# Optimization experiments

Hardware: AMD Instinct MI355X
Metric: run time of the kernel (lower is better)

Reference implementation:

```python
import jax, jax.numpy as jnp
import numpy as np

N, E, G, D, C = 50000, 800000, 512, 128, 10
BN_EPS = 1e-5

def setup_inputs() -> dict:
    key = jax.random.key(0)
    ks = jax.random.split(key, 12)
    inp = {
        'x': jnp.zeros((N,), dtype=jnp.int64 if jax.config.jax_enable_x64 else jnp.int32),
        'edge_index': jax.random.randint(ks[0], (2, E), 0, N),
        'batch_ids': jnp.sort(jax.random.randint(ks[1], (N,), 0, G)),
        'emb': jax.random.normal(ks[2], (1, D), jnp.float32),
        'W1a': jax.random.normal(ks[3], (D, D), jnp.float32) * 0.05,
        'b1a': jnp.zeros((D,), jnp.float32),
        'g1': jnp.ones((D,), jnp.float32),
        'be1': jnp.zeros((D,), jnp.float32),
        'W1b': jax.random.normal(ks[4], (D, D), jnp.float32) * 0.05,
        'b1b': jnp.zeros((D,), jnp.float32),
        'W2a': jax.random.normal(ks[5], (D, D), jnp.float32) * 0.05,
        'b2a': jnp.zeros((D,), jnp.float32),
        'g2': jnp.ones((D,), jnp.float32),
        'be2': jnp.zeros((D,), jnp.float32),
        'W2b': jax.random.normal(ks[6], (D, D), jnp.float32) * 0.05,
        'b2b': jnp.zeros((D,), jnp.float32),
        'Wm': jax.random.normal(ks[7], (D, C), jnp.float32) * 0.05,
        'bm': jnp.zeros((C,), jnp.float32),
        'Wx': jax.random.normal(ks[8], (D, C), jnp.float32) * 0.05,
        'bx': jnp.zeros((C,), jnp.float32),
        'ens_w': jnp.array([0.6, 0.4], jnp.float32),
    }
    return inp

def _gin_layer(h, src, dst, Wa, ba, g, be, Wb, bb):
    # GINConv, eps=0: mlp(x + sum_{j in N(i)} x_j)
    agg = jax.ops.segment_sum(h[src], dst, num_segments=N)  # [N, D]
    z = (h + agg) @ Wa + ba
    mu = jnp.mean(z, axis=0)
    var = jnp.var(z, axis=0)  # biased, as torch BN training forward
    z = (z - mu) * jax.lax.rsqrt(var + BN_EPS) * g + be
    z = jax.nn.relu(z)  # dropout is identity in eval
    return z @ Wb + bb

def reference(x, edge_index, batch_ids, emb, W1a, b1a, g1, be1, W1b, b1b,
              W2a, b2a, g2, be2, W2b, b2b, Wm, bm, Wx, bx, ens_w):
    src, dst = edge_index[0], edge_index[1]
    h0 = emb[x]  # [N, D] (all indices 0)
    h1 = _gin_layer(h0, src, dst, W1a, b1a, g1, be1, W1b, b1b)
    h2 = _gin_layer(h1, src, dst, W2a, b2a, g2, be2, W2b, b2b) + h1
    # global mean / max pooling over batch segments
    counts = jax.ops.segment_sum(jnp.ones((N,), h2.dtype), batch_ids, num_segments=G)
    mean_repr = jax.ops.segment_sum(h2, batch_ids, num_segments=G) / jnp.maximum(counts, 1.0)[:, None]
    max_repr = jax.ops.segment_max(h2, batch_ids, num_segments=G)
    max_repr = jnp.where(jnp.isfinite(max_repr), max_repr, 0.0)  # empty segments -> 0
    logits_mean = mean_repr @ Wm + bm
    logits_max = max_repr @ Wx + bx
    w = jax.nn.softmax(ens_w)
    ensemble_logits = w[0] * logits_mean + w[1] * logits_max
    return (ensemble_logits, logits_mean, logits_max, (mean_repr, max_repr))
```

## Files before the change

### kernel.cpp

```cpp
#include <hip/hip_runtime.h>
#include <math.h>

#define N_NODES  50000
#define N_EDGES  800000
#define N_GRAPHS 512
#define DIM      128
#define NCLS     10
#define KH       64
#define KW       32
#define KT       128
#define OVF_CAP  65536
#define BN_EPS   1e-5f


__global__ void k_zero(uint4* __restrict__ p, long long n4) {
    long long i = (long long)blockIdx.x * blockDim.x + threadIdx.x;
    if (i < n4) p[i] = make_uint4(0u, 0u, 0u, 0u);
}

__global__ void k_count_deg(const int* __restrict__ dst, int* __restrict__ deg) {
    int e = blockIdx.x * blockDim.x + threadIdx.x;
    if (e < N_EDGES) atomicAdd(&deg[dst[e]], 1);
}

__global__ void k_sumdeg2(const int* __restrict__ deg, unsigned long long* __restrict__ sum2) {
    __shared__ unsigned long long lds[256];
    int i = blockIdx.x * blockDim.x + threadIdx.x;
    unsigned long long v = 0;
    if (i < N_NODES) {
        unsigned long long d = (unsigned long long)(unsigned int)deg[i];
        v = d * d;
    }
    lds[threadIdx.x] = v;
    __syncthreads();
    for (int s = blockDim.x >> 1; s > 0; s >>= 1) {
        if ((int)threadIdx.x < s) lds[threadIdx.x] += lds[threadIdx.x + s];
        __syncthreads();
    }
    if (threadIdx.x == 0) atomicAdd(sum2, lds[0]);
}

__device__ inline int lower_bound_i(const int* __restrict__ a, int n, int v) {
    int lo = 0, hi = n;
    while (lo < hi) {
        int mid = (lo + hi) >> 1;
        if (a[mid] < v) lo = mid + 1; else hi = mid;
    }
    return lo;
}

__global__ void k_bounds(const int* __restrict__ batch, int* __restrict__ seg) {
    int g = threadIdx.x;
    if (g < N_GRAPHS) seg[g] = lower_bound_i(batch, N_NODES, g);
    if (g == 0) seg[N_GRAPHS] = N_NODES;
}

__global__ void k_prep(const float* __restrict__ emb, const float* __restrict__ W1a,
                       const float* __restrict__ g1, const float* __restrict__ be1,
                       const unsigned long long* __restrict__ sum2,
                       float* __restrict__ A, float* __restrict__ B) {
    int d = threadIdx.x;
    float u = 0.f;
    for (int k = 0; k < DIM; ++k) u += emb[k] * W1a[k * DIM + d];
    double mdeg = (double)N_EDGES / (double)N_NODES;
    double vdeg = (double)(*sum2) / (double)N_NODES - mdeg * mdeg;
    float var = (float)((double)u * (double)u * vdeg);
    float rs  = rsqrtf(var + BN_EPS);
    float a   = u * rs * g1[d];
    A[d] = a;
    B[d] = be1[d] - (float)mdeg * a;
}

__global__ void k_tables(const float* __restrict__ A, const float* __restrict__ B,
                         const float* __restrict__ W1b, const float* __restrict__ b1b,
                         const float* __restrict__ W2a,
                         float* __restrict__ table, float* __restrict__ table2) {
    int k = blockIdx.x, d = threadIdx.x;
    __shared__ float r[DIM];
    __shared__ float t[DIM];
    float kf = (float)k;
    r[d] = fmaxf(kf * A[d] + B[d], 0.f);
    __syncthreads();
    float acc = b1b[d];
    for (int j = 0; j < DIM; ++j) acc += r[j] * W1b[j * DIM + d];
    table[(size_t)k * DIM + d] = acc;
    t[d] = acc;
    __syncthreads();
    float acc2 = 0.f;
    for (int j = 0; j < DIM; ++j) acc2 += t[j] * W2a[j * DIM + d];
    table2[(size_t)k * DIM + d] = acc2;
}

__global__ void k_edges(const int* __restrict__ src, const int* __restrict__ dst,
                        const int* __restrict__ deg, unsigned int* __restrict__ m,
                        unsigned int* __restrict__ ovf_cnt, int* __restrict__ ovf_buf) {
    int e = blockIdx.x * blockDim.x + threadIdx.x;
    if (e >= N_EDGES) return;
    int s = src[e], dd = dst[e];
    int k = deg[s];
    if (k < KH) {
        atomicAdd(&m[(size_t)dd * KW + (k >> 1)], 1u << ((k & 1) << 4));
    } else {
        unsigned int idx = atomicAdd(ovf_cnt, 1u);
        if (idx < OVF_CAP) {
            ovf_buf[2 * idx] = dd;
            ovf_buf[2 * idx + 1] = k;
        }
    }
}

__global__ __launch_bounds__(256) void k_gemm1(
        const unsigned int* __restrict__ m, const int* __restrict__ deg,
        const float* __restrict__ table2, const float* __restrict__ b2a,
        float* __restrict__ z2, double* __restrict__ colsum, double* __restrict__ colsq,
        const unsigned int* __restrict__ ovf_cnt, const int* __restrict__ ovf_buf) {
    __shared__ __align__(16) unsigned int lds_m[64 * 33];
    const int t = threadIdx.x;
    const int i0 = blockIdx.x * 64;
    #pragma unroll
    for (int q = 0; q < 2; ++q) {
        int idx = t + 256 * q;
        int row = idx >> 3, c = (idx & 7) << 2;
        uint4 v = make_uint4(0u, 0u, 0u, 0u);
        if (i0 + row < N_NODES) v = *(const uint4*)&m[(size_t)(i0 + row) * KW + c];
        lds_m[row * 33 + c + 0] = v.x;
        lds_m[row * 33 + c + 1] = v.y;
        lds_m[row * 33 + c + 2] = v.z;
        lds_m[row * 33 + c + 3] = v.w;
    }
    __syncthreads();

    const int g = t >> 5;
    const int c4 = (t & 31) << 2;
    const int rbase = g * 8;
    float acc[8][4] = {};
    #pragma unroll 4
    for (int w = 0; w < KW; ++w) {
        float4 ta = *(const float4*)&table2[(size_t)(2 * w) * DIM + c4];
        float4 tb = *(const float4*)&table2[(size_t)(2 * w + 1) * DIM + c4];
        #pragma unroll
        for (int r = 0; r < 8; ++r) {
            unsigned int mw = lds_m[(rbase + r) * 33 + w];
            float lo = (float)(mw & 0xFFFFu);
            float hi = (float)(mw >> 16);
            acc[r][0] += lo * ta.x + hi * tb.x;
            acc[r][1] += lo * ta.y + hi * tb.y;
            acc[r][2] += lo * ta.z + hi * tb.z;
            acc[r][3] += lo * ta.w + hi * tb.w;
        }
    }

    unsigned int nov = *ovf_cnt;
    if (nov > OVF_CAP) nov = OVF_CAP;
    for (unsigned int u = 0; u < nov; ++u) {
        int dd = ovf_buf[2 * u];
        int r = dd - i0;
        if (r >= 0 && r < 64 && (r >> 3) == g) {
            int kk = ovf_buf[2 * u + 1]; if (kk > KT - 1) kk = KT - 1;
            float4 tv = *(const float4*)&table2[(size_t)kk * DIM + c4];
            acc[r & 7][0] += tv.x; acc[r & 7][1] += tv.y;
            acc[r & 7][2] += tv.z; acc[r & 7][3] += tv.w;
        }
    }

    float4 bb = *(const float4*)&b2a[c4];
    float s4[4] = {0.f, 0.f, 0.f, 0.f};
    float q4[4] = {0.f, 0.f, 0.f, 0.f};
    #pragma unroll
    for (int r = 0; r < 8; ++r) {
        int row = i0 + rbase + r;
        if (row < N_NODES) {
            int kk = deg[row]; if (kk > KT - 1) kk = KT - 1;
            float4 self = *(const float4*)&table2[(size_t)kk * DIM + c4];
            float v0 = acc[r][0] + self.x + bb.x;
            float v1 = acc[r][1] + self.y + bb.y;
            float v2 = acc[r][2] + self.z + bb.z;
            float v3 = acc[r][3] + self.w + bb.w;
            *(float4*)&z2[(size_t)row * DIM + c4] = make_float4(v0, v1, v2, v3);
            s4[0] += v0; q4[0] += v0 * v0;
            s4[1] += v1; q4[1] += v1 * v1;
            s4[2] += v2; q4[2] += v2 * v2;
            s4[3] += v3; q4[3] += v3 * v3;
        }
    }
    __syncthreads();
    float* red = (float*)lds_m;
    #pragma unroll
    for (int j = 0; j < 4; ++j) {
        red[g * 128 + c4 + j] = s4[j];
        red[1024 + g * 128 + c4 + j] = q4[j];
    }
    __syncthreads();
    if (t < 128) {
        double ss = 0.0, qq = 0.0;
        #pragma unroll
        for (int gg = 0; gg < 8; ++gg) {
            ss += (double)red[gg * 128 + t];
            qq += (double)red[1024 + gg * 128 + t];
        }
        atomicAdd(&colsum[t], ss);
        atomicAdd(&colsq[t], qq);
    }
}

__global__ void k_fin2(const double* __restrict__ colsum, const double* __restrict__ colsq,
                       const float* __restrict__ g2, const float* __restrict__ be2,
                       float* __restrict__ A2, float* __restrict__ B2) {
    int d = threadIdx.x;
    double mu = colsum[d] / (double)N_NODES;
    double var = colsq[d] / (double)N_NODES - mu * mu;
    float rs = rsqrtf((float)var + BN_EPS);
    float a = rs * g2[d];
    A2[d] = a;
    B2[d] = be2[d] - (float)mu * a;
}

__global__ __launch_bounds__(256) void k_gemm2(
        const float* __restrict__ z2, const float* __restrict__ A2, const float* __restrict__ B2,
        const float* __restrict__ W2b, const float* __restrict__ b2b,
        const float* __restrict__ table, const int* __restrict__ deg,
        float* __restrict__ h2) {
    __shared__ __align__(16) float lds_zn[64 * 132];
    const int t = threadIdx.x;
    const int i0 = blockIdx.x * 64;
    #pragma unroll
    for (int q = 0; q < 8; ++q) {
        int idx = t + 256 * q;
        int row = idx >> 5, cc = (idx & 31) << 2;
        float4 zv = make_float4(0.f, 0.f, 0.f, 0.f);
        if (i0 + row < N_NODES) zv = *(const float4*)&z2[(size_t)(i0 + row) * DIM + cc];
        float4 av = *(const float4*)&A2[cc];
        float4 bv = *(const float4*)&B2[cc];
        lds_zn[row * 132 + cc + 0] = fmaxf(zv.x * av.x + bv.x, 0.f);
        lds_zn[row * 132 + cc + 1] = fmaxf(zv.y * av.y + bv.y, 0.f);
        lds_zn[row * 132 + cc + 2] = fmaxf(zv.z * av.z + bv.z, 0.f);
        lds_zn[row * 132 + cc + 3] = fmaxf(zv.w * av.w + bv.w, 0.f);
    }
    __syncthreads();

    const int g = t >> 5;
    const int c4 = (t & 31) << 2;
    const int rbase = g * 8;
    float acc[8][4] = {};
    #pragma unroll 4
    for (int k = 0; k < DIM; ++k) {
        float4 wv = *(const float4*)&W2b[(size_t)k * DIM + c4];
        #pragma unroll
        for (int r = 0; r < 8; ++r) {
            float zv = lds_zn[(rbase + r) * 132 + k];
            acc[r][0] += zv * wv.x;
            acc[r][1] += zv * wv.y;
            acc[r][2] += zv * wv.z;
            acc[r][3] += zv * wv.w;
        }
    }

    float4 bb = *(const float4*)&b2b[c4];
    #pragma unroll
    for (int r = 0; r < 8; ++r) {
        int row = i0 + rbase + r;
        if (row < N_NODES) {
            int kk = deg[row]; if (kk > KT - 1) kk = KT - 1;
            float4 tb = *(const float4*)&table[(size_t)kk * DIM + c4];
            float4 o;
            o.x = acc[r][0] + bb.x + tb.x;
            o.y = acc[r][1] + bb.y + tb.y;
            o.z = acc[r][2] + bb.z + tb.z;
            o.w = acc[r][3] + bb.w + tb.w;
            *(float4*)&h2[(size_t)row * DIM + c4] = o;
        }
    }
}

__global__ __launch_bounds__(1024) void k_pool(
        const float* __restrict__ h2, const int* __restrict__ seg,
        float* __restrict__ out_mean, float* __restrict__ out_max) {
    __shared__ float reds[32 * 132];
    __shared__ float redm[32 * 132];
    int g = blockIdx.x;
    int s0 = seg[g], e0 = seg[g + 1];
    int rg = threadIdx.x >> 5;
    int c4 = (threadIdx.x & 31) << 2;
    float s[4] = {0.f, 0.f, 0.f, 0.f};
    float mx[4] = {-INFINITY, -INFINITY, -INFINITY, -INFINITY};
    for (int i = s0 + rg; i < e0; i += 32) {
        float4 v = *(const float4*)&h2[(size_t)i * DIM + c4];
        s[0] += v.x; mx[0] = fmaxf(mx[0], v.x);
        s[1] += v.y; mx[1] = fmaxf(mx[1], v.y);
        s[2] += v.z; mx[2] = fmaxf(mx[2], v.z);
        s[3] += v.w; mx[3] = fmaxf(mx[3], v.w);
    }
    #pragma unroll
    for (int j = 0; j < 4; ++j) {
        reds[rg * 132 + c4 + j] = s[j];
        redm[rg * 132 + c4 + j] = mx[j];
    }
    __syncthreads();
    for (int step = 16; step >= 1; step >>= 1) {
        if (rg < step) {
            #pragma unroll
            for (int j = 0; j < 4; ++j) {
                reds[rg * 132 + c4 + j] += reds[(rg + step) * 132 + c4 + j];
                redm[rg * 132 + c4 + j] = fmaxf(redm[rg * 132 + c4 + j],
                                                redm[(rg + step) * 132 + c4 + j]);
            }
        }
        __syncthreads();
    }
    if (rg == 0) {
        int cnt = e0 - s0;
        float denom = (float)(cnt > 0 ? cnt : 1);
        #pragma unroll
        for (int j = 0; j < 4; ++j) {
            float sum = reds[c4 + j];
            float mxv = redm[c4 + j];
            out_mean[(size_t)g * DIM + c4 + j] = sum / denom;
            out_max[(size_t)g * DIM + c4 + j]  = (cnt > 0) ? mxv : 0.f;
        }
    }
}

__global__ void k_head(const float* __restrict__ mean_repr, const float* __restrict__ max_repr,
                       const float* __restrict__ Wm, const float* __restrict__ bm,
                       const float* __restrict__ Wx, const float* __restrict__ bx,
                       const float* __restrict__ ensw,
                       float* __restrict__ out_ens, float* __restrict__ out_lm,
                       float* __restrict__ out_lx) {
    int g = blockIdx.x, c = threadIdx.x;
    if (c >= NCLS) return;
    float lm = bm[c], lx = bx[c];
    const float* mr = mean_repr + (size_t)g * DIM;
    const float* xr = max_repr + (size_t)g * DIM;
    for (int d = 0; d < DIM; ++d) {
        lm += mr[d] * Wm[d * NCLS + c];
        lx += xr[d] * Wx[d * NCLS + c];
    }
    float a0 = ensw[0], a1 = ensw[1];
    float mw = fmaxf(a0, a1);
    float e0 = expf(a0 - mw), e1 = expf(a1 - mw);
    float inv = 1.f / (e0 + e1);
    float w0 = e0 * inv, w1 = e1 * inv;
    out_lm[(size_t)g * NCLS + c] = lm;
    out_lx[(size_t)g * NCLS + c] = lx;
    out_ens[(size_t)g * NCLS + c] = w0 * lm + w1 * lx;
}


extern "C" void kernel_launch(void* const* d_in, const int* in_sizes, int n_in,
                              void* d_out, int out_size, void* d_ws, size_t ws_size,
                              hipStream_t stream) {
    const int* edge = (const int*)d_in[1];
    const int* src = edge;
    const int* dst = edge + N_EDGES;
    const int* batch = (const int*)d_in[2];
    const float* emb = (const float*)d_in[3];
    const float* W1a = (const float*)d_in[4];
    const float* g1  = (const float*)d_in[6];
    const float* be1 = (const float*)d_in[7];
    const float* W1b = (const float*)d_in[8];
    const float* b1b = (const float*)d_in[9];
    const float* W2a = (const float*)d_in[10];
    const float* b2a = (const float*)d_in[11];
    const float* g2  = (const float*)d_in[12];
    const float* be2 = (const float*)d_in[13];
    const float* W2b = (const float*)d_in[14];
    const float* b2b = (const float*)d_in[15];
    const float* Wm  = (const float*)d_in[16];
    const float* bm  = (const float*)d_in[17];
    const float* Wx  = (const float*)d_in[18];
    const float* bx  = (const float*)d_in[19];
    const float* ensw = (const float*)d_in[20];

    char* ws = (char*)d_ws;
    size_t off = 0;
    auto take = [&](size_t bytes) {
        char* p = ws + off;
        off += (bytes + 511) & ~(size_t)511;
        return p;
    };
    int* deg                  = (int*)take((size_t)N_NODES * 4);
    unsigned int* m           = (unsigned int*)take((size_t)N_NODES * KW * 4);
    unsigned long long* sum2  = (unsigned long long*)take(8);
    double* colsum            = (double*)take(DIM * 8);
    double* colsq             = (double*)take(DIM * 8);
    unsigned int* ovf_cnt     = (unsigned int*)take(4);
    size_t zbytes = off;
    int* ovf_buf              = (int*)take((size_t)OVF_CAP * 2 * 4);
    float* table              = (float*)take((size_t)KT * DIM * 4);
    float* table2             = (float*)take((size_t)KT * DIM * 4);
    float* A                  = (float*)take(DIM * 4);
    float* B                  = (float*)take(DIM * 4);
    float* A2                 = (float*)take(DIM * 4);
    float* B2                 = (float*)take(DIM * 4);
    int* seg                  = (int*)take((size_t)(N_GRAPHS + 1) * 4);
    float* z2                 = (float*)take((size_t)N_NODES * DIM * 4);
    float* h2                 = (float*)take((size_t)N_NODES * DIM * 4);
    (void)ws_size; (void)in_sizes; (void)n_in; (void)out_size;

    float* out      = (float*)d_out;
    float* out_ens  = out;
    float* out_lm   = out + (size_t)N_GRAPHS * NCLS;
    float* out_lx   = out + 2 * (size_t)N_GRAPHS * NCLS;
    float* out_mean = out + 3 * (size_t)N_GRAPHS * NCLS;
    float* out_max  = out_mean + (size_t)N_GRAPHS * DIM;

    long long n4 = (long long)(zbytes >> 4);
    k_zero<<<(int)((n4 + 255) / 256), 256, 0, stream>>>((uint4*)ws, n4);
    k_count_deg<<<(N_EDGES + 255) / 256, 256, 0, stream>>>(dst, deg);
    k_bounds<<<1, N_GRAPHS, 0, stream>>>(batch, seg);
    k_sumdeg2<<<(N_NODES + 255) / 256, 256, 0, stream>>>(deg, sum2);
    k_prep<<<1, DIM, 0, stream>>>(emb, W1a, g1, be1, sum2, A, B);
    k_tables<<<KT, DIM, 0, stream>>>(A, B, W1b, b1b, W2a, table, table2);
    k_edges<<<(N_EDGES + 255) / 256, 256, 0, stream>>>(src, dst, deg, m, ovf_cnt, ovf_buf);
    k_gemm1<<<(N_NODES + 63) / 64, 256, 0, stream>>>(m, deg, table2, b2a, z2,
                                                     colsum, colsq, ovf_cnt, ovf_buf);
    k_fin2<<<1, DIM, 0, stream>>>(colsum, colsq, g2, be2, A2, B2);
    k_gemm2<<<(N_NODES + 63) / 64, 256, 0, stream>>>(z2, A2, B2, W2b, b2b, table, deg, h2);
    k_pool<<<N_GRAPHS, 1024, 0, stream>>>(h2, seg, out_mean, out_max);
    k_head<<<N_GRAPHS, 64, 0, stream>>>(out_mean, out_max, Wm, bm, Wx, bx, ensw,
                                        out_ens, out_lm, out_lx);
}
```

Measured before the change: 188.4 us.

## Replace global atomics with per-block partials and stage degree table in LDS

```diff
diff --git a/kernel.cpp b/kernel.cpp
--- a/kernel.cpp
+++ b/kernel.cpp
@@ -12,6 +12,9 @@
 #define OVF_CAP  65536
 #define BN_EPS   1e-5f
 
+#define NB_GEMM  ((N_NODES + 63) / 64)
+#define NB_DEG   ((N_NODES + 255) / 256)
+
 
 __global__ void k_zero(uint4* __restrict__ p, long long n4) {
     long long i = (long long)blockIdx.x * blockDim.x + threadIdx.x;
@@ -23,7 +26,7 @@
     if (e < N_EDGES) atomicAdd(&deg[dst[e]], 1);
 }
 
-__global__ void k_sumdeg2(const int* __restrict__ deg, unsigned long long* __restrict__ sum2) {
+__global__ void k_sumdeg2(const int* __restrict__ deg, unsigned long long* __restrict__ dpart) {
     __shared__ unsigned long long lds[256];
     int i = blockIdx.x * blockDim.x + threadIdx.x;
     unsigned long long v = 0;
@@ -37,7 +40,7 @@
         if ((int)threadIdx.x < s) lds[threadIdx.x] += lds[threadIdx.x + s];
         __syncthreads();
     }
-    if (threadIdx.x == 0) atomicAdd(sum2, lds[0]);
+    if (threadIdx.x == 0) dpart[blockIdx.x] = lds[0];
 }
 
 __device__ inline int lower_bound_i(const int* __restrict__ a, int n, int v) {
@@ -57,13 +60,16 @@
 
 __global__ void k_prep(const float* __restrict__ emb, const float* __restrict__ W1a,
                        const float* __restrict__ g1, const float* __restrict__ be1,
-                       const unsigned long long* __restrict__ sum2,
+                       const unsigned long long* __restrict__ dpart,
                        float* __restrict__ A, float* __restrict__ B) {
     int d = threadIdx.x;
     float u = 0.f;
     for (int k = 0; k < DIM; ++k) u += emb[k] * W1a[k * DIM + d];
+    unsigned long long s2 = 0;
+    #pragma unroll 4
+    for (int b = 0; b < NB_DEG; ++b) s2 += dpart[b];
     double mdeg = (double)N_EDGES / (double)N_NODES;
-    double vdeg = (double)(*sum2) / (double)N_NODES - mdeg * mdeg;
+    double vdeg = (double)s2 / (double)N_NODES - mdeg * mdeg;
     float var = (float)((double)u * (double)u * vdeg);
     float rs  = rsqrtf(var + BN_EPS);
     float a   = u * rs * g1[d];
@@ -112,11 +118,18 @@
 __global__ __launch_bounds__(256) void k_gemm1(
         const unsigned int* __restrict__ m, const int* __restrict__ deg,
         const float* __restrict__ table2, const float* __restrict__ b2a,
-        float* __restrict__ z2, double* __restrict__ colsum, double* __restrict__ colsq,
+        float* __restrict__ z2, float* __restrict__ spart,
         const unsigned int* __restrict__ ovf_cnt, const int* __restrict__ ovf_buf) {
+    __shared__ __align__(16) float lds_t2[64 * 128];
     __shared__ __align__(16) unsigned int lds_m[64 * 33];
     const int t = threadIdx.x;
     const int i0 = blockIdx.x * 64;
+    #pragma unroll
+    for (int q = 0; q < 8; ++q) {
+        int idx = t + 256 * q;
+        int row = idx >> 5, c = (idx & 31) << 2;
+        *(float4*)&lds_t2[row * 128 + c] = *(const float4*)&table2[(size_t)row * 128 + c];
+    }
     #pragma unroll
     for (int q = 0; q < 2; ++q) {
         int idx = t + 256 * q;
@@ -136,8 +149,8 @@
     float acc[8][4] = {};
     #pragma unroll 4
     for (int w = 0; w < KW; ++w) {
-        float4 ta = *(const float4*)&table2[(size_t)(2 * w) * DIM + c4];
-        float4 tb = *(const float4*)&table2[(size_t)(2 * w + 1) * DIM + c4];
+        float4 ta = *(const float4*)&lds_t2[(2 * w) * 128 + c4];
+        float4 tb = *(const float4*)&lds_t2[(2 * w + 1) * 128 + c4];
         #pragma unroll
         for (int r = 0; r < 8; ++r) {
             unsigned int mw = lds_m[(rbase + r) * 33 + w];
@@ -170,8 +183,13 @@
     for (int r = 0; r < 8; ++r) {
         int row = i0 + rbase + r;
         if (row < N_NODES) {
-            int kk = deg[row]; if (kk > KT - 1) kk = KT - 1;
-            float4 self = *(const float4*)&table2[(size_t)kk * DIM + c4];
+            int kk = deg[row];
+            float4 self;
+            if (kk < KH) self = *(const float4*)&lds_t2[kk * 128 + c4];
+            else {
+                if (kk > KT - 1) kk = KT - 1;
+                self = *(const float4*)&table2[(size_t)kk * DIM + c4];
+            }
             float v0 = acc[r][0] + self.x + bb.x;
             float v1 = acc[r][1] + self.y + bb.y;
             float v2 = acc[r][2] + self.z + bb.z;
@@ -192,27 +210,41 @@
     }
     __syncthreads();
     if (t < 128) {
-        double ss = 0.0, qq = 0.0;
+        float ss = 0.f, qq = 0.f;
         #pragma unroll
         for (int gg = 0; gg < 8; ++gg) {
-            ss += (double)red[gg * 128 + t];
-            qq += (double)red[1024 + gg * 128 + t];
-        }
-        atomicAdd(&colsum[t], ss);
-        atomicAdd(&colsq[t], qq);
-    }
-}
-
-__global__ void k_fin2(const double* __restrict__ colsum, const double* __restrict__ colsq,
-                       const float* __restrict__ g2, const float* __restrict__ be2,
-                       float* __restrict__ A2, float* __restrict__ B2) {
-    int d = threadIdx.x;
-    double mu = colsum[d] / (double)N_NODES;
-    double var = colsq[d] / (double)N_NODES - mu * mu;
-    float rs = rsqrtf((float)var + BN_EPS);
-    float a = rs * g2[d];
-    A2[d] = a;
-    B2[d] = be2[d] - (float)mu * a;
+            ss += red[gg * 128 + t];
+            qq += red[1024 + gg * 128 + t];
+        }
+        spart[(size_t)blockIdx.x * 256 + t] = ss;
+        spart[(size_t)blockIdx.x * 256 + 128 + t] = qq;
+    }
+}
+
+__global__ __launch_bounds__(1024) void k_fin2(
+        const float* __restrict__ spart,
+        const float* __restrict__ g2, const float* __restrict__ be2,
+        float* __restrict__ A2, float* __restrict__ B2) {
+    __shared__ double red[4 * 256];
+    int t = threadIdx.x & 255;
+    int q = threadIdx.x >> 8;
+    double acc = 0.0;
+    #pragma unroll 4
+    for (int b = q; b < NB_GEMM; b += 4) acc += (double)spart[(size_t)b * 256 + t];
+    red[q * 256 + t] = acc;
+    __syncthreads();
+    if (threadIdx.x < 256)
+        red[threadIdx.x] = red[threadIdx.x] + red[256 + threadIdx.x] +
+                           red[512 + threadIdx.x] + red[768 + threadIdx.x];
+    __syncthreads();
+    if (threadIdx.x < 128) {
+        double mu = red[threadIdx.x] / (double)N_NODES;
+        double var = red[128 + threadIdx.x] / (double)N_NODES - mu * mu;
+        float rs = rsqrtf((float)var + BN_EPS);
+        float a = rs * g2[threadIdx.x];
+        A2[threadIdx.x] = a;
+        B2[threadIdx.x] = be2[threadIdx.x] - (float)mu * a;
+    }
 }
 
 __global__ __launch_bounds__(256) void k_gemm2(
@@ -242,20 +274,35 @@
     const int c4 = (t & 31) << 2;
     const int rbase = g * 8;
     float acc[8][4] = {};
-    #pragma unroll 4
-    for (int k = 0; k < DIM; ++k) {
-        float4 wv = *(const float4*)&W2b[(size_t)k * DIM + c4];
+    float4 wa[4], wb[4];
+    #pragma unroll
+    for (int j = 0; j < 4; ++j)
+        wa[j] = *(const float4*)&W2b[(size_t)j * DIM + c4];
+    #pragma unroll 2
+    for (int kb = 0; kb < 32; ++kb) {
+        const float4* cur = (kb & 1) ? wb : wa;
+        float4* nxt = (kb & 1) ? wa : wb;
+        if (kb < 31) {
+            #pragma unroll
+            for (int j = 0; j < 4; ++j)
+                nxt[j] = *(const float4*)&W2b[(size_t)((kb + 1) * 4 + j) * DIM + c4];
+        }
         #pragma unroll
-        for (int r = 0; r < 8; ++r) {
-            float zv = lds_zn[(rbase + r) * 132 + k];
-            acc[r][0] += zv * wv.x;
-            acc[r][1] += zv * wv.y;
-            acc[r][2] += zv * wv.z;
-            acc[r][3] += zv * wv.w;
-        }
-    }
-
-    float4 bb = *(const float4*)&b2b[c4];
+        for (int j = 0; j < 4; ++j) {
+            int k = kb * 4 + j;
+            float4 wv = cur[j];
+            #pragma unroll
+            for (int r = 0; r < 8; ++r) {
+                float zv = lds_zn[(rbase + r) * 132 + k];
+                acc[r][0] += zv * wv.x;
+                acc[r][1] += zv * wv.y;
+                acc[r][2] += zv * wv.z;
+                acc[r][3] += zv * wv.w;
+            }
+        }
+    }
+
+    float4 bbv = *(const float4*)&b2b[c4];
     #pragma unroll
     for (int r = 0; r < 8; ++r) {
         int row = i0 + rbase + r;
@@ -263,10 +310,10 @@
             int kk = deg[row]; if (kk > KT - 1) kk = KT - 1;
             float4 tb = *(const float4*)&table[(size_t)kk * DIM + c4];
             float4 o;
-            o.x = acc[r][0] + bb.x + tb.x;
-            o.y = acc[r][1] + bb.y + tb.y;
-            o.z = acc[r][2] + bb.z + tb.z;
-            o.w = acc[r][3] + bb.w + tb.w;
+            o.x = acc[r][0] + bbv.x + tb.x;
+            o.y = acc[r][1] + bbv.y + tb.y;
+            o.z = acc[r][2] + bbv.z + tb.z;
+            o.w = acc[r][3] + bbv.w + tb.w;
             *(float4*)&h2[(size_t)row * DIM + c4] = o;
         }
     }
@@ -380,11 +427,10 @@
     };
     int* deg                  = (int*)take((size_t)N_NODES * 4);
     unsigned int* m           = (unsigned int*)take((size_t)N_NODES * KW * 4);
-    unsigned long long* sum2  = (unsigned long long*)take(8);
-    double* colsum            = (double*)take(DIM * 8);
-    double* colsq             = (double*)take(DIM * 8);
     unsigned int* ovf_cnt     = (unsigned int*)take(4);
     size_t zbytes = off;
+    unsigned long long* dpart = (unsigned long long*)take((size_t)NB_DEG * 8);
+    float* spart              = (float*)take((size_t)NB_GEMM * 256 * 4);
     int* ovf_buf              = (int*)take((size_t)OVF_CAP * 2 * 4);
     float* table              = (float*)take((size_t)KT * DIM * 4);
     float* table2             = (float*)take((size_t)KT * DIM * 4);
@@ -408,14 +454,13 @@
     k_zero<<<(int)((n4 + 255) / 256), 256, 0, stream>>>((uint4*)ws, n4);
     k_count_deg<<<(N_EDGES + 255) / 256, 256, 0, stream>>>(dst, deg);
     k_bounds<<<1, N_GRAPHS, 0, stream>>>(batch, seg);
-    k_sumdeg2<<<(N_NODES + 255) / 256, 256, 0, stream>>>(deg, sum2);
-    k_prep<<<1, DIM, 0, stream>>>(emb, W1a, g1, be1, sum2, A, B);
+    k_sumdeg2<<<NB_DEG, 256, 0, stream>>>(deg, dpart);
+    k_prep<<<1, DIM, 0, stream>>>(emb, W1a, g1, be1, dpart, A, B);
     k_tables<<<KT, DIM, 0, stream>>>(A, B, W1b, b1b, W2a, table, table2);
     k_edges<<<(N_EDGES + 255) / 256, 256, 0, stream>>>(src, dst, deg, m, ovf_cnt, ovf_buf);
-    k_gemm1<<<(N_NODES + 63) / 64, 256, 0, stream>>>(m, deg, table2, b2a, z2,
-                                                     colsum, colsq, ovf_cnt, ovf_buf);
-    k_fin2<<<1, DIM, 0, stream>>>(colsum, colsq, g2, be2, A2, B2);
-    k_gemm2<<<(N_NODES + 63) / 64, 256, 0, stream>>>(z2, A2, B2, W2b, b2b, table, deg, h2);
+    k_gemm1<<<NB_GEMM, 256, 0, stream>>>(m, deg, table2, b2a, z2, spart, ovf_cnt, ovf_buf);
+    k_fin2<<<1, 1024, 0, stream>>>(spart, g2, be2, A2, B2);
+    k_gemm2<<<NB_GEMM, 256, 0, stream>>>(z2, A2, B2, W2b, b2b, table, deg, h2);
     k_pool<<<N_GRAPHS, 1024, 0, stream>>>(h2, seg, out_mean, out_max);
     k_head<<<N_GRAPHS, 64, 0, stream>>>(out_mean, out_max, Wm, bm, Wx, bx, ensw,
                                         out_ens, out_lm, out_lx);
```

Result: slower. 201.4 us (+6.9%).
